# Optimization experiments

Hardware: AMD Instinct MI355X
Metric: run time of the kernel (lower is better)

Reference implementation:

```python
import jax, jax.numpy as jnp
import numpy as np

BETA = 0.25


def setup_inputs() -> dict:
    key = jax.random.key(0)
    k1, k2 = jax.random.split(key)
    x = jax.random.normal(k1, (32, 32, 32, 256), dtype=jnp.float32)
    codebook = jax.random.normal(k2, (1024, 256), dtype=jnp.float32)
    return {"x": x, "codebook": codebook}


def reference(x, codebook):
    D = codebook.shape[1]
    z_fla = x.reshape(-1, D)  # [N, D]
    # squared euclidean distances [N, K]
    dis = (jnp.sum(z_fla ** 2, axis=1, keepdims=True)
           + jnp.sum(codebook ** 2, axis=1)
           - 2.0 * jnp.matmul(z_fla, codebook.T))
    min_encoding_indices = jnp.argmin(dis, axis=1)  # [N] int
    z_q = codebook[min_encoding_indices].reshape(x.shape)
    loss = (jnp.mean((jax.lax.stop_gradient(z_q) - x) ** 2)
            + BETA * jnp.mean((z_q - jax.lax.stop_gradient(x)) ** 2))
    z_q = x + jax.lax.stop_gradient(z_q - x)  # straight-through
    # faithful to source: mean of the index values, then "perplexity" formula
    e_min = jnp.mean(min_encoding_indices.astype(jnp.float32), axis=0)
    perplexity = jnp.exp(-jnp.sum(e_min * jnp.log(e_min + 1e-10)))
    return (loss, z_q, perplexity, min_encoding_indices)
```

## Files before the change

kernel.cpp:

```cpp
#include <hip/hip_runtime.h>
#include <cmath>

#define NROWS 32768
#define DDIM  256
#define KCB   1024

constexpr float TAU = 0.25f;
constexpr int BSTR = 264;

typedef _Float16 half8 __attribute__((ext_vector_type(8)));
typedef float floatx4 __attribute__((ext_vector_type(4)));

__global__ void init_kernel(double* __restrict__ sumsq, int* __restrict__ sumidx,
                            unsigned* __restrict__ done2, int* __restrict__ nfull) {
  *sumsq = 0.0; *sumidx = 0; *done2 = 0u; *nfull = 0;
}

__global__ __launch_bounds__(64) void prep_kernel(const float* __restrict__ cb,
                                                  float* __restrict__ cn) {
  const int k = blockIdx.x, lane = threadIdx.x;
  float4 v = *(const float4*)(cb + (size_t)k * DDIM + lane * 4);
  double s = (double)v.x * v.x + (double)v.y * v.y
           + (double)v.z * v.z + (double)v.w * v.w;
  #pragma unroll
  for (int off = 32; off; off >>= 1) s += __shfl_down(s, off);
  if (lane == 0) cn[k] = (float)s;
}

__global__ __launch_bounds__(512, 2) void fused_kernel(
    const float* __restrict__ x,
    const float* __restrict__ cb,
    const float* __restrict__ cn,
    float* __restrict__ zq_out,
    float* __restrict__ idx_out,
    double* __restrict__ sumsq,
    int* __restrict__ sumidx,
    int* __restrict__ nfull_g,
    int* __restrict__ glist) {
  __shared__ __align__(16) _Float16 bs[2][64 * BSTR];
  __shared__ float cn_lds[KCB];
  __shared__ int   bidx[128];
  __shared__ int   bidx2[128];
  __shared__ float m2s[128];
  __shared__ float m3s[128];
  __shared__ int   plist[128];
  __shared__ int   npair;
  __shared__ float wred[8];

  const int tid = threadIdx.x;
  const int lane = tid & 63;
  const int w = tid >> 6;
  const int q = lane >> 4;
  const int tx = lane & 15;
  const int row0 = blockIdx.x * 128;

  half8 a_hi[8], a_lo[8];
  {
    const float* xp = x + (size_t)(row0 + w * 16 + tx) * DDIM + q * 8;
    #pragma unroll
    for (int s = 0; s < 8; ++s) {
      float4 v0 = *(const float4*)(xp + s * 32);
      float4 v1 = *(const float4*)(xp + s * 32 + 4);
      half8 h, l;
      _Float16 t;
      t = (_Float16)v0.x; h[0] = t; l[0] = (_Float16)(v0.x - (float)t);
      t = (_Float16)v0.y; h[1] = t; l[1] = (_Float16)(v0.y - (float)t);
      t = (_Float16)v0.z; h[2] = t; l[2] = (_Float16)(v0.z - (float)t);
      t = (_Float16)v0.w; h[3] = t; l[3] = (_Float16)(v0.w - (float)t);
      t = (_Float16)v1.x; h[4] = t; l[4] = (_Float16)(v1.x - (float)t);
      t = (_Float16)v1.y; h[5] = t; l[5] = (_Float16)(v1.y - (float)t);
      t = (_Float16)v1.z; h[6] = t; l[6] = (_Float16)(v1.z - (float)t);
      t = (_Float16)v1.w; h[7] = t; l[7] = (_Float16)(v1.w - (float)t);
      a_hi[s] = h; a_lo[s] = l;
    }
  }
  cn_lds[tid] = cn[tid];
  cn_lds[tid + 512] = cn[tid + 512];
  if (tid == 0) npair = 0;

  float4 vld[8];
  auto load_stage = [&](int ct) {
    #pragma unroll
    for (int i = 0; i < 4; ++i) {
      int p = tid + 512 * i;
      const float* src = cb + (size_t)ct * 16384 + (size_t)p * 8;
      vld[2 * i]     = *(const float4*)src;
      vld[2 * i + 1] = *(const float4*)(src + 4);
    }
  };
  auto write_stage = [&](int buf) {
    #pragma unroll
    for (int i = 0; i < 4; ++i) {
      int p = tid + 512 * i;
      int e = p >> 5, c = p & 31;
      float4 v0 = vld[2 * i], v1 = vld[2 * i + 1];
      half8 h;
      h[0] = (_Float16)v0.x; h[1] = (_Float16)v0.y;
      h[2] = (_Float16)v0.z; h[3] = (_Float16)v0.w;
      h[4] = (_Float16)v1.x; h[5] = (_Float16)v1.y;
      h[6] = (_Float16)v1.z; h[7] = (_Float16)v1.w;
      *(half8*)&bs[buf][e * BSTR + c * 8] = h;
    }
  };

  float v1[4], v2[4], v3[4];
  int i1[4], i2[4];
  #pragma unroll
  for (int r = 0; r < 4; ++r) {
    v1[r] = INFINITY; v2[r] = INFINITY; v3[r] = INFINITY; i1[r] = 0; i2[r] = 0;
  }

  load_stage(0);
  for (int st = 0; st < 16; ++st) {
    const int buf = st & 1;
    write_stage(buf);
    __syncthreads();
    if (st + 1 < 16) load_stage(st + 1);

    floatx4 ahh[4], alh[4];
    #pragma unroll
    for (int ci = 0; ci < 4; ++ci) {
      ahh[ci] = (floatx4){0.f, 0.f, 0.f, 0.f};
      alh[ci] = (floatx4){0.f, 0.f, 0.f, 0.f};
    }

    #pragma unroll
    for (int s = 0; s < 8; ++s) {
      #pragma unroll
      for (int ci = 0; ci < 4; ++ci) {
        half8 bh = *(const half8*)&bs[buf][(ci * 16 + tx) * BSTR + (s * 4 + q) * 8];
        ahh[ci] = __builtin_amdgcn_mfma_f32_16x16x32_f16(a_hi[s], bh, ahh[ci], 0, 0, 0);
        alh[ci] = __builtin_amdgcn_mfma_f32_16x16x32_f16(a_lo[s], bh, alh[ci], 0, 0, 0);
      }
    }

    #pragma unroll
    for (int ci = 0; ci < 4; ++ci) {
      int col = st * 64 + ci * 16 + tx;
      float cnv = cn_lds[col];
      #pragma unroll
      for (int r = 0; r < 4; ++r) {
        float dot = ahh[ci][r] + alh[ci][r];
        float dist = cnv - 2.f * dot;
        if (dist < v1[r]) {
          v3[r] = v2[r]; v2[r] = v1[r]; i2[r] = i1[r];
          v1[r] = dist; i1[r] = col;
        } else if (dist < v2[r]) {
          v3[r] = v2[r]; v2[r] = dist; i2[r] = col;
        } else if (dist < v3[r]) {
          v3[r] = dist;
        }
      }
    }
  }

  #pragma unroll
  for (int off = 8; off; off >>= 1) {
    #pragma unroll
    for (int r = 0; r < 4; ++r) {
      float ov1 = __shfl_down(v1[r], off, 16);
      int   oi1 = __shfl_down(i1[r], off, 16);
      float ov2 = __shfl_down(v2[r], off, 16);
      int   oi2 = __shfl_down(i2[r], off, 16);
      float ov3 = __shfl_down(v3[r], off, 16);
      bool takeo = (ov1 < v1[r]) || (ov1 == v1[r] && oi1 < i1[r]);
      float n1v = takeo ? ov1 : v1[r];
      int   n1i = takeo ? oi1 : i1[r];
      float l1 = takeo ? v1[r] : v2[r];
      int   l1i = takeo ? i1[r] : i2[r];
      float l2 = takeo ? v2[r] : v3[r];
      float r1 = takeo ? ov2 : ov1;
      int   r1i = takeo ? oi2 : oi1;
      float r2 = takeo ? ov3 : ov2;
      bool t2 = (r1 < l1) || (r1 == l1 && r1i < l1i);
      float n2v = t2 ? r1 : l1;
      int   n2i = t2 ? r1i : l1i;
      float n3v = t2 ? fminf(r2, l1) : fminf(l2, r1);
      v1[r] = n1v; i1[r] = n1i; v2[r] = n2v; i2[r] = n2i; v3[r] = n3v;
    }
  }
  if (tx == 0) {
    #pragma unroll
    for (int r = 0; r < 4; ++r) {
      int R = w * 16 + q * 4 + r;
      bidx[R]  = i1[r];
      bidx2[R] = i2[r];
      m2s[R] = v2[r] - v1[r];
      m3s[R] = v3[r] - v1[r];
    }
  }
  __syncthreads();

  if (tid < 128) {
    if (m3s[tid] < TAU) {
      int p = atomicAdd(nfull_g, 1);
      glist[p] = row0 + tid;
    } else if (m2s[tid] < TAU) {
      int p = atomicAdd(&npair, 1);
      plist[p] = tid;
    }
  }
  __syncthreads();

  for (int f = w; f < npair; f += 8) {
    int r = plist[f];
    int cA = bidx[r], cB = bidx2[r];
    int c = (lane >= 32) ? cB : cA;
    int ld = lane & 31;
    const float* xp = x  + (size_t)(row0 + r) * DDIM + ld * 8;
    const float* cp = cb + (size_t)c * DDIM + ld * 8;
    double s = 0.0;
    #pragma unroll
    for (int j = 0; j < 8; j += 4) {
      float4 xv = *(const float4*)(xp + j);
      float4 cv = *(const float4*)(cp + j);
      double d0 = (double)xv.x - (double)cv.x; s = fma(d0, d0, s);
      double d1 = (double)xv.y - (double)cv.y; s = fma(d1, d1, s);
      double d2 = (double)xv.z - (double)cv.z; s = fma(d2, d2, s);
      double d3 = (double)xv.w - (double)cv.w; s = fma(d3, d3, s);
    }
    #pragma unroll
    for (int off = 16; off; off >>= 1) s += __shfl_xor(s, off);
    double dA = __shfl(s, 0), dB = __shfl(s, 32);
    if (lane == 0) {
      bool takeB = (dB < dA) || (dB == dA && cB < cA);
      bidx[r] = takeB ? cB : cA;
    }
  }
  __syncthreads();

  if (tid < 128) idx_out[row0 + tid] = (float)bidx[tid];

  float lsum = 0.f;
  #pragma unroll 4
  for (int it = 0; it < 16; ++it) {
    int g = tid + 512 * it;
    int r = g >> 6;
    int c4 = (g & 63) << 2;
    int k = bidx[r] & (KCB - 1);
    float4 cv = *(const float4*)(cb + (size_t)k * DDIM + c4);
    float4 xv = *(const float4*)(x + (size_t)(row0 + r) * DDIM + c4);
    float d0 = cv.x - xv.x, d1 = cv.y - xv.y, d2 = cv.z - xv.z, d3 = cv.w - xv.w;
    lsum = fmaf(d0, d0, lsum); lsum = fmaf(d1, d1, lsum);
    lsum = fmaf(d2, d2, lsum); lsum = fmaf(d3, d3, lsum);
    *(float4*)(zq_out + (size_t)(row0 + r) * DDIM + c4) = cv;
  }
  #pragma unroll
  for (int off = 32; off; off >>= 1) lsum += __shfl_down(lsum, off);
  if (lane == 0) wred[w] = lsum;
  __syncthreads();
  if (tid == 0) {
    double ls = 0.0;
    #pragma unroll
    for (int ww = 0; ww < 8; ++ww) ls += (double)wred[ww];
    atomicAdd(sumsq, ls);
    int si = 0;
    #pragma unroll 8
    for (int r = 0; r < 128; ++r) si += bidx[r] & (KCB - 1);
    atomicAdd(sumidx, si);
  }
}

__global__ __launch_bounds__(256) void cleanup_kernel(
    const float* __restrict__ x,
    const float* __restrict__ cb,
    float* __restrict__ zq_out,
    float* __restrict__ idx_out,
    float* __restrict__ out_loss,
    float* __restrict__ out_perp,
    double* __restrict__ sumsq,
    int* __restrict__ sumidx,
    const int* __restrict__ nfull_g,
    const int* __restrict__ glist,
    unsigned* __restrict__ done2) {
  __shared__ __align__(16) float xr[DDIM];
  __shared__ double rv[4];
  __shared__ int    ri[4];
  __shared__ double dold_s;
  __shared__ int    kstar_s;

  const int tid = threadIdx.x;
  const int lane = tid & 63;
  const int w = tid >> 6;
  const int nitems = *nfull_g;

  for (int it = blockIdx.x; it < nitems; it += gridDim.x) {
    int row = glist[it];
    int kold = (int)idx_out[row];
    __syncthreads();
    if (tid < 64) {
      float4 v = *(const float4*)(x + (size_t)row * DDIM + tid * 4);
      xr[tid * 4 + 0] = v.x; xr[tid * 4 + 1] = v.y;
      xr[tid * 4 + 2] = v.z; xr[tid * 4 + 3] = v.w;
    }
    __syncthreads();
    double bd = 1e300; int bi = 0;
    #pragma unroll
    for (int j = 0; j < 4; ++j) {
      int c = tid * 4 + j;
      const float* cp = cb + (size_t)c * DDIM;
      double s0 = 0.0, s1 = 0.0, s2 = 0.0, s3 = 0.0;
      for (int d = 0; d < DDIM; d += 4) {
        float4 cv = *(const float4*)(cp + d);
        float4 xv = *(const float4*)&xr[d];
        double d0 = (double)xv.x - (double)cv.x; s0 = fma(d0, d0, s0);
        double d1 = (double)xv.y - (double)cv.y; s1 = fma(d1, d1, s1);
        double d2 = (double)xv.z - (double)cv.z; s2 = fma(d2, d2, s2);
        double d3 = (double)xv.w - (double)cv.w; s3 = fma(d3, d3, s3);
      }
      double s = (s0 + s1) + (s2 + s3);
      if (s < bd) { bd = s; bi = c; }
      if (c == kold) dold_s = s;
    }
    #pragma unroll
    for (int off = 32; off; off >>= 1) {
      double ov = __shfl_down(bd, off);
      int oi = __shfl_down(bi, off);
      if (ov < bd || (ov == bd && oi < bi)) { bd = ov; bi = oi; }
    }
    if (lane == 0) { rv[w] = bd; ri[w] = bi; }
    __syncthreads();
    if (tid == 0) {
      double bv = rv[0]; int bix = ri[0];
      #pragma unroll
      for (int ww = 1; ww < 4; ++ww)
        if (rv[ww] < bv || (rv[ww] == bv && ri[ww] < bix)) { bv = rv[ww]; bix = ri[ww]; }
      if (bix != kold) {
        idx_out[row] = (float)bix;
        atomicAdd(sumsq, bv - dold_s);
        atomicAdd(sumidx, bix - kold);
      }
      kstar_s = bix;
    }
    __syncthreads();
    int kst = kstar_s;
    if (kst != kold)
      zq_out[(size_t)row * DDIM + tid] = cb[(size_t)kst * DDIM + tid];
  }

  __syncthreads();
  if (tid == 0) {
    __threadfence();
    unsigned prev = atomicAdd(done2, 1u);
    if (prev == gridDim.x - 1) {
      __threadfence();
      double ss = atomicAdd(sumsq, 0.0);
      int    sidx = atomicAdd(sumidx, 0);
      double loss = 1.25 * ss / 8388608.0;
      double e_min = (double)sidx / 32768.0;
      double perp = exp(-e_min * log(e_min + 1e-10));
      *out_loss = (float)loss;
      *out_perp = (float)perp;
    }
  }
}

extern "C" void kernel_launch(void* const* d_in, const int* in_sizes, int n_in,
                              void* d_out, int out_size, void* d_ws, size_t ws_size,
                              hipStream_t stream) {
  const float* x  = (const float*)d_in[0];
  const float* cb = (const float*)d_in[1];
  float* out = (float*)d_out;
  float* out_loss = out;
  float* out_zq   = out + 1;
  float* out_perp = out + 1 + 8388608;
  float* out_idx  = out + 2 + 8388608;

  double*   sumsq  = (double*)d_ws;
  int*      sumidx = (int*)((char*)d_ws + 8);
  unsigned* done2  = (unsigned*)((char*)d_ws + 12);
  int*      nfull  = (int*)((char*)d_ws + 16);
  float*    cn     = (float*)((char*)d_ws + 64);
  int*      glist  = (int*)((char*)d_ws + 8192);

  hipLaunchKernelGGL(init_kernel, dim3(1), dim3(1), 0, stream,
                     sumsq, sumidx, done2, nfull);
  hipLaunchKernelGGL(prep_kernel, dim3(KCB), dim3(64), 0, stream, cb, cn);
  hipLaunchKernelGGL(fused_kernel, dim3(NROWS / 128), dim3(512), 0, stream,
                     x, cb, cn, out_zq, out_idx, sumsq, sumidx, nfull, glist);
  hipLaunchKernelGGL(cleanup_kernel, dim3(256), dim3(256), 0, stream,
                     x, cb, out_zq, out_idx, out_loss, out_perp,
                     sumsq, sumidx, nfull, glist, done2);
}
```

Measured before the change: 181.7 us.

## Pre-convert codebook to fp16, shrink blocks to 64 rows, fold init into prep

The prep kernel now also writes an fp16 copy of the codebook to workspace and zeroes the accumulators, which removes the separate init launch. The fused kernel streams the fp16 codebook in 32-column stages instead of converting fp32 tiles each stage, which halves the bytes loaded per stage and removes the convert work. Blocks shrink from 512 to 256 threads covering 64 rows, so there are twice as many blocks. In exchange, the codebook is read from global memory by twice as many blocks and each block runs twice as many barrier-synchronised stages. An fp32 fallback path is kept for when the workspace is too small.

```diff
diff --git a/kernel.cpp b/kernel.cpp
--- a/kernel.cpp
+++ b/kernel.cpp
@@ -9,17 +9,26 @@
 constexpr int BSTR = 264;
 
 typedef _Float16 half8 __attribute__((ext_vector_type(8)));
+typedef _Float16 half4 __attribute__((ext_vector_type(4)));
 typedef float floatx4 __attribute__((ext_vector_type(4)));
 
-__global__ void init_kernel(double* __restrict__ sumsq, int* __restrict__ sumidx,
-                            unsigned* __restrict__ done2, int* __restrict__ nfull) {
-  *sumsq = 0.0; *sumidx = 0; *done2 = 0u; *nfull = 0;
-}
-
+template<bool CVT>
 __global__ __launch_bounds__(64) void prep_kernel(const float* __restrict__ cb,
-                                                  float* __restrict__ cn) {
+                                                  float* __restrict__ cn,
+                                                  _Float16* __restrict__ cbh,
+                                                  double* __restrict__ sumsq,
+                                                  int* __restrict__ sumidx,
+                                                  unsigned* __restrict__ done2,
+                                                  int* __restrict__ nfull) {
   const int k = blockIdx.x, lane = threadIdx.x;
+  if (k == 0 && lane == 0) { *sumsq = 0.0; *sumidx = 0; *done2 = 0u; *nfull = 0; }
   float4 v = *(const float4*)(cb + (size_t)k * DDIM + lane * 4);
+  if constexpr (CVT) {
+    half4 h;
+    h[0] = (_Float16)v.x; h[1] = (_Float16)v.y;
+    h[2] = (_Float16)v.z; h[3] = (_Float16)v.w;
+    *(half4*)&cbh[(size_t)k * DDIM + lane * 4] = h;
+  }
   double s = (double)v.x * v.x + (double)v.y * v.y
            + (double)v.z * v.z + (double)v.w * v.w;
   #pragma unroll
@@ -27,9 +36,11 @@
   if (lane == 0) cn[k] = (float)s;
 }
 
-__global__ __launch_bounds__(512, 2) void fused_kernel(
+template<bool H>
+__global__ __launch_bounds__(256, 2) void fused_kernel(
     const float* __restrict__ x,
     const float* __restrict__ cb,
+    const _Float16* __restrict__ cbh,
     const float* __restrict__ cn,
     float* __restrict__ zq_out,
     float* __restrict__ idx_out,
@@ -37,22 +48,22 @@
     int* __restrict__ sumidx,
     int* __restrict__ nfull_g,
     int* __restrict__ glist) {
-  __shared__ __align__(16) _Float16 bs[2][64 * BSTR];
+  __shared__ __align__(16) _Float16 bs[2][32 * BSTR];
   __shared__ float cn_lds[KCB];
-  __shared__ int   bidx[128];
-  __shared__ int   bidx2[128];
-  __shared__ float m2s[128];
-  __shared__ float m3s[128];
-  __shared__ int   plist[128];
+  __shared__ int   bidx[64];
+  __shared__ int   bidx2[64];
+  __shared__ float m2s[64];
+  __shared__ float m3s[64];
+  __shared__ int   plist[64];
   __shared__ int   npair;
-  __shared__ float wred[8];
+  __shared__ float wred[4];
 
   const int tid = threadIdx.x;
   const int lane = tid & 63;
   const int w = tid >> 6;
   const int q = lane >> 4;
   const int tx = lane & 15;
-  const int row0 = blockIdx.x * 128;
+  const int row0 = blockIdx.x * 64;
 
   half8 a_hi[8], a_lo[8];
   {
@@ -74,32 +85,41 @@
       a_hi[s] = h; a_lo[s] = l;
     }
   }
-  cn_lds[tid] = cn[tid];
-  cn_lds[tid + 512] = cn[tid + 512];
+  #pragma unroll
+  for (int i = 0; i < 4; ++i) cn_lds[tid + 256 * i] = cn[tid + 256 * i];
   if (tid == 0) npair = 0;
 
-  float4 vld[8];
+  half8 vld[4];
+  float4 vldf[8];
   auto load_stage = [&](int ct) {
     #pragma unroll
     for (int i = 0; i < 4; ++i) {
-      int p = tid + 512 * i;
-      const float* src = cb + (size_t)ct * 16384 + (size_t)p * 8;
-      vld[2 * i]     = *(const float4*)src;
-      vld[2 * i + 1] = *(const float4*)(src + 4);
+      int u = tid + 256 * i;
+      if constexpr (H) {
+        vld[i] = *(const half8*)&cbh[(size_t)ct * 8192 + (size_t)u * 8];
+      } else {
+        const float* src = cb + (size_t)ct * 8192 + (size_t)u * 8;
+        vldf[2 * i]     = *(const float4*)src;
+        vldf[2 * i + 1] = *(const float4*)(src + 4);
+      }
     }
   };
   auto write_stage = [&](int buf) {
     #pragma unroll
     for (int i = 0; i < 4; ++i) {
-      int p = tid + 512 * i;
-      int e = p >> 5, c = p & 31;
-      float4 v0 = vld[2 * i], v1 = vld[2 * i + 1];
-      half8 h;
-      h[0] = (_Float16)v0.x; h[1] = (_Float16)v0.y;
-      h[2] = (_Float16)v0.z; h[3] = (_Float16)v0.w;
-      h[4] = (_Float16)v1.x; h[5] = (_Float16)v1.y;
-      h[6] = (_Float16)v1.z; h[7] = (_Float16)v1.w;
-      *(half8*)&bs[buf][e * BSTR + c * 8] = h;
+      int u = tid + 256 * i;
+      int e = u >> 5, c = u & 31;
+      if constexpr (H) {
+        *(half8*)&bs[buf][e * BSTR + c * 8] = vld[i];
+      } else {
+        float4 v0 = vldf[2 * i], v1 = vldf[2 * i + 1];
+        half8 h;
+        h[0] = (_Float16)v0.x; h[1] = (_Float16)v0.y;
+        h[2] = (_Float16)v0.z; h[3] = (_Float16)v0.w;
+        h[4] = (_Float16)v1.x; h[5] = (_Float16)v1.y;
+        h[6] = (_Float16)v1.z; h[7] = (_Float16)v1.w;
+        *(half8*)&bs[buf][e * BSTR + c * 8] = h;
+      }
     }
   };
 
@@ -111,15 +131,15 @@
   }
 
   load_stage(0);
-  for (int st = 0; st < 16; ++st) {
+  for (int st = 0; st < 32; ++st) {
     const int buf = st & 1;
     write_stage(buf);
     __syncthreads();
-    if (st + 1 < 16) load_stage(st + 1);
-
-    floatx4 ahh[4], alh[4];
-    #pragma unroll
-    for (int ci = 0; ci < 4; ++ci) {
+    if (st + 1 < 32) load_stage(st + 1);
+
+    floatx4 ahh[2], alh[2];
+    #pragma unroll
+    for (int ci = 0; ci < 2; ++ci) {
       ahh[ci] = (floatx4){0.f, 0.f, 0.f, 0.f};
       alh[ci] = (floatx4){0.f, 0.f, 0.f, 0.f};
     }
@@ -127,7 +147,7 @@
     #pragma unroll
     for (int s = 0; s < 8; ++s) {
       #pragma unroll
-      for (int ci = 0; ci < 4; ++ci) {
+      for (int ci = 0; ci < 2; ++ci) {
         half8 bh = *(const half8*)&bs[buf][(ci * 16 + tx) * BSTR + (s * 4 + q) * 8];
         ahh[ci] = __builtin_amdgcn_mfma_f32_16x16x32_f16(a_hi[s], bh, ahh[ci], 0, 0, 0);
         alh[ci] = __builtin_amdgcn_mfma_f32_16x16x32_f16(a_lo[s], bh, alh[ci], 0, 0, 0);
@@ -135,8 +155,8 @@
     }
 
     #pragma unroll
-    for (int ci = 0; ci < 4; ++ci) {
-      int col = st * 64 + ci * 16 + tx;
+    for (int ci = 0; ci < 2; ++ci) {
+      int col = st * 32 + ci * 16 + tx;
       float cnv = cn_lds[col];
       #pragma unroll
       for (int r = 0; r < 4; ++r) {
@@ -191,7 +211,7 @@
   }
   __syncthreads();
 
-  if (tid < 128) {
+  if (tid < 64) {
     if (m3s[tid] < TAU) {
       int p = atomicAdd(nfull_g, 1);
       glist[p] = row0 + tid;
@@ -202,7 +222,7 @@
   }
   __syncthreads();
 
-  for (int f = w; f < npair; f += 8) {
+  for (int f = w; f < npair; f += 4) {
     int r = plist[f];
     int cA = bidx[r], cB = bidx2[r];
     int c = (lane >= 32) ? cB : cA;
@@ -229,12 +249,12 @@
   }
   __syncthreads();
 
-  if (tid < 128) idx_out[row0 + tid] = (float)bidx[tid];
+  if (tid < 64) idx_out[row0 + tid] = (float)bidx[tid];
 
   float lsum = 0.f;
   #pragma unroll 4
   for (int it = 0; it < 16; ++it) {
-    int g = tid + 512 * it;
+    int g = tid + 256 * it;
     int r = g >> 6;
     int c4 = (g & 63) << 2;
     int k = bidx[r] & (KCB - 1);
@@ -250,13 +270,12 @@
   if (lane == 0) wred[w] = lsum;
   __syncthreads();
   if (tid == 0) {
-    double ls = 0.0;
-    #pragma unroll
-    for (int ww = 0; ww < 8; ++ww) ls += (double)wred[ww];
+    double ls = (double)wred[0] + (double)wred[1]
+              + (double)wred[2] + (double)wred[3];
     atomicAdd(sumsq, ls);
     int si = 0;
     #pragma unroll 8
-    for (int r = 0; r < 128; ++r) si += bidx[r] & (KCB - 1);
+    for (int r = 0; r < 64; ++r) si += bidx[r] & (KCB - 1);
     atomicAdd(sumidx, si);
   }
 }
@@ -371,13 +390,24 @@
   unsigned* done2  = (unsigned*)((char*)d_ws + 12);
   int*      nfull  = (int*)((char*)d_ws + 16);
   float*    cn     = (float*)((char*)d_ws + 64);
-  int*      glist  = (int*)((char*)d_ws + 8192);
-
-  hipLaunchKernelGGL(init_kernel, dim3(1), dim3(1), 0, stream,
-                     sumsq, sumidx, done2, nfull);
-  hipLaunchKernelGGL(prep_kernel, dim3(KCB), dim3(64), 0, stream, cb, cn);
-  hipLaunchKernelGGL(fused_kernel, dim3(NROWS / 128), dim3(512), 0, stream,
-                     x, cb, cn, out_zq, out_idx, sumsq, sumidx, nfull, glist);
+  _Float16* cbh    = (_Float16*)((char*)d_ws + 8192);
+  int*      glistH = (int*)((char*)d_ws + 8192 + 524288);
+  int*      glistL = (int*)((char*)d_ws + 8192);
+
+  const bool useH = ws_size >= (size_t)(8192 + 524288 + 131072);
+  int* glist = useH ? glistH : glistL;
+
+  if (useH) {
+    hipLaunchKernelGGL(prep_kernel<true>, dim3(KCB), dim3(64), 0, stream,
+                       cb, cn, cbh, sumsq, sumidx, done2, nfull);
+    hipLaunchKernelGGL(fused_kernel<true>, dim3(NROWS / 64), dim3(256), 0, stream,
+                       x, cb, cbh, cn, out_zq, out_idx, sumsq, sumidx, nfull, glist);
+  } else {
+    hipLaunchKernelGGL(prep_kernel<false>, dim3(KCB), dim3(64), 0, stream,
+                       cb, cn, cbh, sumsq, sumidx, done2, nfull);
+    hipLaunchKernelGGL(fused_kernel<false>, dim3(NROWS / 64), dim3(256), 0, stream,
+                       x, cb, cbh, cn, out_zq, out_idx, sumsq, sumidx, nfull, glist);
+  }
   hipLaunchKernelGGL(cleanup_kernel, dim3(256), dim3(256), 0, stream,
                      x, cb, out_zq, out_idx, out_loss, out_perp,
                      sumsq, sumidx, nfull, glist, done2);
```

Measured after the change: 177.5 us. 2.3% less time.
